# Kernel tuning notes

Hardware: AMD Instinct MI355X
Metric: run time of the kernel (lower is better)

The kernel has to match this reference:

```python
import jax, jax.numpy as jnp
import numpy as np

LN_EPS = 1e-5
L2_EPS = 1e-12
SCALE = 8.0

def setup_inputs() -> dict:
    key = jax.random.key(0)
    k0, k1, k2 = jax.random.split(key, 3)
    b, c, H, W = 16, 256, 64, 64
    heads, dim_head = 8, 32
    dim_inner = heads * dim_head  # 256
    x = jax.random.normal(k0, (b, c, H, W), dtype=jnp.float32)
    ln_gamma = jnp.ones((c,), jnp.float32)
    ln_beta = jnp.zeros((c,), jnp.float32)
    W_qkv = jax.random.normal(k1, (c, 3 * dim_inner), dtype=jnp.float32) * 0.02
    temperature = jnp.ones((heads,), jnp.float32)
    W_out = jax.random.normal(k2, (dim_inner, c), dtype=jnp.float32) * 0.02
    b_out = jnp.zeros((c,), jnp.float32)
    return {"x": x, "ln_gamma": ln_gamma, "ln_beta": ln_beta, "W_qkv": W_qkv,
            "temperature": temperature, "W_out": W_out, "b_out": b_out, "heads": heads}

def _l2norm(t):
    # F.normalize(t, dim=-1): divide by clamped L2 norm along last axis
    n = jnp.sqrt(jnp.sum(t * t, axis=-1, keepdims=True))
    return t / jnp.maximum(n, L2_EPS)

def reference(x, ln_gamma, ln_beta, W_qkv, temperature, W_out, b_out, heads):
    b, c, H, W = x.shape
    n = H * W
    dim_head = W_qkv.shape[1] // (3 * heads)
    # b c h w -> b (h w) c
    t = jnp.transpose(x, (0, 2, 3, 1)).reshape(b, n, c)
    # LayerNorm over channel dim (affine)
    mu = jnp.mean(t, axis=-1, keepdims=True)
    var = jnp.mean(jnp.square(t - mu), axis=-1, keepdims=True)
    t = (t - mu) * jax.lax.rsqrt(var + LN_EPS) * ln_gamma + ln_beta
    # qkv projection; split last dim as (qkv, heads, dim_head) -> (3, b, h, d, n)
    qkv = (t @ W_qkv).reshape(b, n, 3, heads, dim_head)
    qkv = jnp.transpose(qkv, (2, 0, 3, 4, 1))
    q, k, v = qkv[0], qkv[1], qkv[2]
    q = _l2norm(q) * jnp.exp(temperature)[None, :, None, None]
    k = _l2norm(k)
    # cross-covariance attention over channel dim: sim is [b, h, d, d]
    sim = jnp.einsum('bhin,bhjn->bhij', q, k) * SCALE
    attn = jax.nn.softmax(sim, axis=-1)
    out = jnp.einsum('bhij,bhjn->bhin', attn, v)  # [b, h, d, n]
    # b h d n -> b n (h d)
    out = jnp.transpose(out, (0, 3, 1, 2)).reshape(b, n, heads * dim_head)
    out = out @ W_out + b_out
    # b (h w) c -> b c h w
    return jnp.transpose(out.reshape(b, H, W, c), (0, 3, 1, 2))
```

## Files before the change

### kernel.cpp

```cpp
#include <hip/hip_runtime.h>

typedef unsigned short u16;
typedef __bf16 bf16x8 __attribute__((ext_vector_type(8)));
typedef float f32x4 __attribute__((ext_vector_type(4)));

#define MFMA(a, b, c) __builtin_amdgcn_mfma_f32_16x16x32_bf16((a), (b), (c), 0, 0, 0)

__device__ __forceinline__ u16 f2bf(float f) {
    unsigned u = __float_as_uint(f);
    unsigned r = (u + 0x7fffu + ((u >> 16) & 1u)) >> 16;
    return (u16)r;
}
__device__ __forceinline__ float bf2f(u16 h) { return __uint_as_float(((unsigned)h) << 16); }

typedef unsigned int u32_g __attribute__((address_space(1)));
typedef unsigned int u32_l __attribute__((address_space(3)));
__device__ __forceinline__ void gload16(const void* g, void* l) {
    __builtin_amdgcn_global_load_lds((const u32_g*)g, (u32_l*)l, 16, 0, 0);
}


__global__ __launch_bounds__(256) void k_ln(const float* __restrict__ x,
                                            const float* __restrict__ gamma,
                                            const float* __restrict__ beta,
                                            u16* __restrict__ xlnT, u16* __restrict__ xcn) {
    int bid = blockIdx.x;
    int b = bid >> 7, nt = bid & 127;
    int nb = nt * 32;
    __shared__ float redS[32 * 17], redS2[32 * 17];
    __shared__ float muv[32], rsv[32];
    __shared__ float gs[256], es[256];
    __shared__ unsigned xst[256 * 17];
    int t = threadIdx.x;
    int np = t & 15, cg = t >> 4;
    gs[t] = gamma[t];
    es[t] = beta[t];
    const float* xp = x + ((size_t)(b * 256 + cg * 16)) * 4096 + nb + np * 2;
    float2 v[16];
    float s0 = 0.f, s1 = 0.f, s20 = 0.f, s21 = 0.f;
#pragma unroll
    for (int i = 0; i < 16; i++) {
        float2 f = *(const float2*)(xp + (size_t)i * 4096);
        v[i] = f;
        s0 += f.x; s20 += f.x * f.x;
        s1 += f.y; s21 += f.y * f.y;
    }
    redS[(2 * np) * 17 + cg] = s0;
    redS[(2 * np + 1) * 17 + cg] = s1;
    redS2[(2 * np) * 17 + cg] = s20;
    redS2[(2 * np + 1) * 17 + cg] = s21;
    __syncthreads();
    if (t < 32) {
        float s = 0.f, s2 = 0.f;
#pragma unroll
        for (int g = 0; g < 16; g++) { s += redS[t * 17 + g]; s2 += redS2[t * 17 + g]; }
        float m = s * (1.f / 256.f);
        float var = s2 * (1.f / 256.f) - m * m;
        muv[t] = m;
        rsv[t] = rsqrtf(var + 1e-5f);
    }
    __syncthreads();
    float m0 = muv[2 * np], r0 = rsv[2 * np];
    float m1 = muv[2 * np + 1], r1 = rsv[2 * np + 1];
    u16 hA[16], hB[16];
#pragma unroll
    for (int i = 0; i < 16; i++) {
        float g = gs[cg * 16 + i], e = es[cg * 16 + i];
        float a = (v[i].x - m0) * r0 * g + e;
        float c2 = (v[i].y - m1) * r1 * g + e;
        u16 ha = f2bf(a), hb = f2bf(c2);
        hA[i] = ha; hB[i] = hb;
        xst[(cg * 16 + i) * 17 + np] = (unsigned)ha | ((unsigned)hb << 16);
    }
    {
        u16* dst0 = xlnT + ((size_t)(b * 4096 + nb + 2 * np)) * 256 + cg * 16;
        uint4 qa, qb;
        qa.x = (unsigned)hA[0] | ((unsigned)hA[1] << 16);
        qa.y = (unsigned)hA[2] | ((unsigned)hA[3] << 16);
        qa.z = (unsigned)hA[4] | ((unsigned)hA[5] << 16);
        qa.w = (unsigned)hA[6] | ((unsigned)hA[7] << 16);
        qb.x = (unsigned)hA[8] | ((unsigned)hA[9] << 16);
        qb.y = (unsigned)hA[10] | ((unsigned)hA[11] << 16);
        qb.z = (unsigned)hA[12] | ((unsigned)hA[13] << 16);
        qb.w = (unsigned)hA[14] | ((unsigned)hA[15] << 16);
        *(uint4*)dst0 = qa;
        *(uint4*)(dst0 + 8) = qb;
        u16* dst1 = dst0 + 256;
        qa.x = (unsigned)hB[0] | ((unsigned)hB[1] << 16);
        qa.y = (unsigned)hB[2] | ((unsigned)hB[3] << 16);
        qa.z = (unsigned)hB[4] | ((unsigned)hB[5] << 16);
        qa.w = (unsigned)hB[6] | ((unsigned)hB[7] << 16);
        qb.x = (unsigned)hB[8] | ((unsigned)hB[9] << 16);
        qb.y = (unsigned)hB[10] | ((unsigned)hB[11] << 16);
        qb.z = (unsigned)hB[12] | ((unsigned)hB[13] << 16);
        qb.w = (unsigned)hB[14] | ((unsigned)hB[15] << 16);
        *(uint4*)dst1 = qa;
        *(uint4*)(dst1 + 8) = qb;
    }
    __syncthreads();
#pragma unroll
    for (int j = 0; j < 4; j++) {
        int row = (t >> 2) + j * 64, part = t & 3;
        uint4 q;
        q.x = xst[row * 17 + part * 4 + 0];
        q.y = xst[row * 17 + part * 4 + 1];
        q.z = xst[row * 17 + part * 4 + 2];
        q.w = xst[row * 17 + part * 4 + 3];
        *(uint4*)(xcn + ((size_t)(b * 256 + row)) * 4096 + nb + part * 8) = q;
    }
}

__global__ __launch_bounds__(256) void k_prep(const float* __restrict__ Wqkv,
                                              const float* __restrict__ Wout,
                                              u16* __restrict__ WqkvT, u16* __restrict__ WvTn,
                                              u16* __restrict__ WoutT) {
    int i = blockIdx.x * 256 + threadIdx.x;
    if (i < 512 * 256) { int o = i >> 8, c = i & 255; WqkvT[i] = f2bf(Wqkv[c * 768 + o]); }
    if (i < 256 * 256) {
        int e = i >> 8, o = i & 255;
        WvTn[i] = f2bf(Wqkv[e * 768 + 512 + o]);
        WoutT[i] = f2bf(Wout[o * 256 + e]);
    }
}

__global__ __launch_bounds__(256) void k_gram(const u16* __restrict__ xcn, float* __restrict__ Gp) {
    int bid = blockIdx.x;
    int s = bid & 7, tile = (bid >> 3) & 3, b = bid >> 5;
    int tm = tile >> 1, tn = tile & 1;
    __shared__ __align__(16) u16 aT[128 * 32];
    __shared__ __align__(16) u16 bT[128 * 32];
    int t = threadIdx.x, w = t >> 6, lane = t & 63, l15 = lane & 15, quad = lane >> 4;
    int srow = lane >> 2;
    int g8 = (((lane & 3) ^ ((lane >> 3) & 3)) << 3);
    const u16* xb = xcn + (size_t)b * 256 * 4096 + (size_t)s * 512;
    const u16* gA = xb + (size_t)(tm * 128 + w * 32 + srow) * 4096 + g8;
    const u16* gB = xb + (size_t)(tn * 128 + w * 32 + srow) * 4096 + g8;
    u16* lA = aT + w * 1024;
    u16* lB = bT + w * 1024;
    int cOff = ((quad ^ ((l15 >> 1) & 3)) << 3);
    f32x4 acc[2][8];
    f32x4 z = {0.f, 0.f, 0.f, 0.f};
    for (int fm = 0; fm < 2; fm++)
        for (int fn = 0; fn < 8; fn++) acc[fm][fn] = z;
    for (int kt = 0; kt < 16; kt++) {
        int kb = kt * 32;
        if (kt) __syncthreads();
        gload16(gA + kb, lA);
        gload16(gA + 16 * 4096 + kb, lA + 512);
        gload16(gB + kb, lB);
        gload16(gB + 16 * 4096 + kb, lB + 512);
        __syncthreads();
        bf16x8 af0 = *(const bf16x8*)&aT[(w * 32 + l15) * 32 + cOff];
        bf16x8 af1 = *(const bf16x8*)&aT[(w * 32 + 16 + l15) * 32 + cOff];
        for (int fn = 0; fn < 8; fn++) {
            bf16x8 bfr = *(const bf16x8*)&bT[(fn * 16 + l15) * 32 + cOff];
            acc[0][fn] = MFMA(af0, bfr, acc[0][fn]);
            acc[1][fn] = MFMA(af1, bfr, acc[1][fn]);
        }
    }
    float* gp = Gp + (size_t)(s * 16 + b) * 65536;
    for (int fm = 0; fm < 2; fm++)
        for (int fn = 0; fn < 8; fn++)
            for (int r = 0; r < 4; r++) {
                int row = tm * 128 + w * 32 + fm * 16 + quad * 4 + r;
                int col = tn * 128 + fn * 16 + l15;
                gp[row * 256 + col] = acc[fm][fn][r];
            }
}

__global__ __launch_bounds__(256) void k_g2b(const float* __restrict__ Gp,
                                             u16* __restrict__ Ghi, u16* __restrict__ Glo) {
    int idx = blockIdx.x * 256 + threadIdx.x;
    const float4* p = (const float4*)Gp + idx;
    float4 s = p[0];
#pragma unroll
    for (int j = 1; j < 8; j++) {
        float4 v = p[(size_t)j * 262144];
        s.x += v.x; s.y += v.y; s.z += v.z; s.w += v.w;
    }
    u16 h0 = f2bf(s.x), h1 = f2bf(s.y), h2 = f2bf(s.z), h3 = f2bf(s.w);
    u16 l0 = f2bf(s.x - bf2f(h0)), l1 = f2bf(s.y - bf2f(h1));
    u16 l2 = f2bf(s.z - bf2f(h2)), l3 = f2bf(s.w - bf2f(h3));
    uint2 ph; ph.x = (unsigned)h0 | ((unsigned)h1 << 16); ph.y = (unsigned)h2 | ((unsigned)h3 << 16);
    uint2 pl; pl.x = (unsigned)l0 | ((unsigned)l1 << 16); pl.y = (unsigned)l2 | ((unsigned)l3 << 16);
    *(uint2*)(Ghi + (size_t)idx * 4) = ph;
    *(uint2*)(Glo + (size_t)idx * 4) = pl;
}

__global__ __launch_bounds__(256) void k_sq(const u16* __restrict__ A,
                                            const u16* __restrict__ Ghi, const u16* __restrict__ Glo,
                                            u16* __restrict__ Shi, u16* __restrict__ Slo) {
    __shared__ __align__(16) u16 aT[128 * 32];
    __shared__ __align__(16) u16 bT[128 * 32];
    int bid = blockIdx.x;
    int b = bid >> 3;
    int r2 = bid & 7;
    int mbase = (r2 >> 1) * 128, nbase = (r2 & 1) * 128;
    int t = threadIdx.x, w = t >> 6, lane = t & 63, l15 = lane & 15, quad = lane >> 4;
    int srow = lane >> 2;
    int g8 = (((lane & 3) ^ ((lane >> 3) & 3)) << 3);
    const u16* gA = A + (size_t)(mbase + w * 32 + srow) * 256 + g8;
    const u16* gBh = Ghi + (size_t)b * 65536 + (size_t)(nbase + w * 32 + srow) * 256 + g8;
    const u16* gBl = Glo + (size_t)b * 65536 + (size_t)(nbase + w * 32 + srow) * 256 + g8;
    u16* lA = aT + w * 1024;
    u16* lB = bT + w * 1024;
    int cOff = ((quad ^ ((l15 >> 1) & 3)) << 3);
    f32x4 acc[2][8];
    f32x4 z = {0.f, 0.f, 0.f, 0.f};
    for (int fm = 0; fm < 2; fm++)
        for (int fn = 0; fn < 8; fn++) acc[fm][fn] = z;
    for (int kt = 0; kt < 16; kt++) {
        int kb = (kt & 7) * 32;
        const u16* gB = (kt < 8) ? gBh : gBl;
        if (kt) __syncthreads();
        gload16(gA + kb, lA);
        gload16(gA + 16 * 256 + kb, lA + 512);
        gload16(gB + kb, lB);
        gload16(gB + 16 * 256 + kb, lB + 512);
        __syncthreads();
        bf16x8 af0 = *(const bf16x8*)&aT[(w * 32 + l15) * 32 + cOff];
        bf16x8 af1 = *(const bf16x8*)&aT[(w * 32 + 16 + l15) * 32 + cOff];
        for (int fn = 0; fn < 8; fn++) {
            bf16x8 bfr = *(const bf16x8*)&bT[(fn * 16 + l15) * 32 + cOff];
            acc[0][fn] = MFMA(af0, bfr, acc[0][fn]);
            acc[1][fn] = MFMA(af1, bfr, acc[1][fn]);
        }
    }
    for (int fm = 0; fm < 2; fm++)
        for (int fn = 0; fn < 8; fn++)
            for (int r = 0; r < 4; r++) {
                int row = mbase + w * 32 + fm * 16 + quad * 4 + r;
                int col = nbase + fn * 16 + l15;
                float v = acc[fm][fn][r];
                u16 hi = f2bf(v);
                Shi[((size_t)b * 512 + row) * 256 + col] = hi;
                Slo[((size_t)b * 512 + row) * 256 + col] = f2bf(v - bf2f(hi));
            }
}

__global__ __launch_bounds__(256) void k_gemm(const u16* __restrict__ A, size_t aStrB,
                                              const u16* __restrict__ Bb, size_t bStrB,
                                              int mtiles, int ntiles,
                                              u16* __restrict__ o16, float* __restrict__ o32,
                                              const float* __restrict__ bias,
                                              size_t oStrB, int oRstr, int mode) {
    __shared__ __align__(16) u16 aT[128 * 32];
    __shared__ __align__(16) u16 bT[128 * 32];
    int bid = blockIdx.x;
    int per_b = mtiles * ntiles;
    int b = bid / per_b;
    int r2 = bid % per_b;
    int mbase = (r2 / ntiles) * 128, nbase = (r2 % ntiles) * 128;
    int t = threadIdx.x, w = t >> 6, lane = t & 63, l15 = lane & 15, quad = lane >> 4;
    const u16* Ap = A + (size_t)b * aStrB;
    const u16* Bp = Bb + (size_t)b * bStrB;
    int srow = lane >> 2;
    int g8 = (((lane & 3) ^ ((lane >> 3) & 3)) << 3);
    const u16* gA = Ap + (size_t)(mbase + w * 32 + srow) * 256 + g8;
    const u16* gB = Bp + (size_t)(nbase + w * 32 + srow) * 256 + g8;
    u16* lA = aT + w * 1024;
    u16* lB = bT + w * 1024;
    int cOff = ((quad ^ ((l15 >> 1) & 3)) << 3);
    f32x4 acc[2][8];
    f32x4 z = {0.f, 0.f, 0.f, 0.f};
    for (int fm = 0; fm < 2; fm++)
        for (int fn = 0; fn < 8; fn++) acc[fm][fn] = z;
    for (int kt = 0; kt < 8; kt++) {
        int kb = kt * 32;
        if (kt) __syncthreads();
        gload16(gA + kb, lA);
        gload16(gA + 16 * 256 + kb, lA + 512);
        gload16(gB + kb, lB);
        gload16(gB + 16 * 256 + kb, lB + 512);
        __syncthreads();
        bf16x8 af0 = *(const bf16x8*)&aT[(w * 32 + l15) * 32 + cOff];
        bf16x8 af1 = *(const bf16x8*)&aT[(w * 32 + 16 + l15) * 32 + cOff];
        for (int fn = 0; fn < 8; fn++) {
            bf16x8 bfr = *(const bf16x8*)&bT[(fn * 16 + l15) * 32 + cOff];
            acc[0][fn] = MFMA(af0, bfr, acc[0][fn]);
            acc[1][fn] = MFMA(af1, bfr, acc[1][fn]);
        }
    }
    if (mode == 0) {
        for (int fm = 0; fm < 2; fm++)
            for (int fn = 0; fn < 8; fn++)
                for (int r = 0; r < 4; r++) {
                    int row = mbase + w * 32 + fm * 16 + quad * 4 + r;
                    int col = nbase + fn * 16 + l15;
                    o16[(size_t)b * oStrB + (size_t)row * oRstr + col] = f2bf(acc[fm][fn][r]);
                }
    } else {
        for (int fm = 0; fm < 2; fm++)
            for (int fn = 0; fn < 8; fn++)
                for (int r = 0; r < 4; r++) {
                    int row = mbase + w * 32 + fm * 16 + quad * 4 + r;
                    int col = nbase + fn * 16 + l15;
                    o32[(size_t)b * oStrB + (size_t)row * oRstr + col] = acc[fm][fn][r] + bias[row];
                }
    }
}

__global__ __launch_bounds__(256) void k_attn(const u16* __restrict__ Shi,
                                              const u16* __restrict__ Slo,
                                              const u16* __restrict__ WqkvT,
                                              const u16* __restrict__ WoutT,
                                              const float* __restrict__ temp,
                                              u16* __restrict__ M_all) {
    int bh = blockIdx.x;
    int b = bh >> 3, h = bh & 7;
    __shared__ u16 sqh[32 * 264], sql[32 * 264], skh[32 * 264], wq[32 * 264], wk[32 * 264];
    __shared__ u16 wo[256 * 40];
    __shared__ u16 attnT[32 * 40];
    __shared__ float simS[32 * 33];
    __shared__ float redn[4 * 64];
    __shared__ float scq[32], sck[32];
    int t = threadIdx.x, w = t >> 6, lane = t & 63, l15 = lane & 15, quad = lane >> 4;
    {
        int r = t >> 3, cc0 = (t & 7) * 32;
        const u16* gqh = Shi + ((size_t)(b * 512) + h * 32 + r) * 256 + cc0;
        const u16* gql = Slo + ((size_t)(b * 512) + h * 32 + r) * 256 + cc0;
        const u16* gkh = Shi + ((size_t)(b * 512) + 256 + h * 32 + r) * 256 + cc0;
        const u16* gwq = WqkvT + (size_t)(h * 32 + r) * 256 + cc0;
        const u16* gwk = WqkvT + (size_t)(256 + h * 32 + r) * 256 + cc0;
#pragma unroll
        for (int k = 0; k < 4; k++) {
            *(uint4*)&sqh[r * 264 + cc0 + k * 8] = *(const uint4*)(gqh + k * 8);
            *(uint4*)&sql[r * 264 + cc0 + k * 8] = *(const uint4*)(gql + k * 8);
            *(uint4*)&skh[r * 264 + cc0 + k * 8] = *(const uint4*)(gkh + k * 8);
            *(uint4*)&wq[r * 264 + cc0 + k * 8] = *(const uint4*)(gwq + k * 8);
            *(uint4*)&wk[r * 264 + cc0 + k * 8] = *(const uint4*)(gwk + k * 8);
        }
        const u16* gwo = WoutT + (size_t)t * 256 + h * 32;
#pragma unroll
        for (int k = 0; k < 4; k++) *(uint4*)&wo[t * 40 + k * 8] = *(const uint4*)(gwo + k * 8);
    }
    __syncthreads();
    {
        int rn = t & 63, cc = t >> 6;
        int e0 = cc * 64;
        float s = 0.f;
        if (rn < 32) {
            const u16* ph = &sqh[rn * 264];
            const u16* pl = &sql[rn * 264];
            const u16* pb = &wq[rn * 264];
            for (int e = 0; e < 64; e++)
                s += (bf2f(ph[e0 + e]) + bf2f(pl[e0 + e])) * bf2f(pb[e0 + e]);
        } else {
            const u16* ph = &skh[(rn - 32) * 264];
            const u16* pb = &wk[(rn - 32) * 264];
            for (int e = 0; e < 64; e++)
                s += bf2f(ph[e0 + e]) * bf2f(pb[e0 + e]);
        }
        redn[cc * 64 + rn] = s;
    }
    {
        int iq = w >> 1, jq = w & 1;
        f32x4 acc = {0.f, 0.f, 0.f, 0.f};
        for (int s8 = 0; s8 < 8; s8++) {
            bf16x8 a = *(const bf16x8*)&sqh[(iq * 16 + l15) * 264 + s8 * 32 + quad * 8];
            bf16x8 bb = *(const bf16x8*)&wk[(jq * 16 + l15) * 264 + s8 * 32 + quad * 8];
            acc = MFMA(a, bb, acc);
        }
        for (int s8 = 0; s8 < 8; s8++) {
            bf16x8 a = *(const bf16x8*)&sql[(iq * 16 + l15) * 264 + s8 * 32 + quad * 8];
            bf16x8 bb = *(const bf16x8*)&wk[(jq * 16 + l15) * 264 + s8 * 32 + quad * 8];
            acc = MFMA(a, bb, acc);
        }
        for (int r = 0; r < 4; r++)
            simS[(iq * 16 + quad * 4 + r) * 33 + jq * 16 + l15] = acc[r];
    }
    __syncthreads();
    if (t < 32)
        scq[t] = expf(temp[h]) * 8.0f /
                 fmaxf(sqrtf(redn[t] + redn[64 + t] + redn[128 + t] + redn[192 + t]), 1e-12f);
    else if (t < 64) {
        int d = t - 32;
        sck[d] = 1.0f / fmaxf(sqrtf(redn[32 + d] + redn[96 + d] + redn[160 + d] + redn[224 + d]), 1e-12f);
    }
    __syncthreads();
    if (t < 32) {
        float row[32];
        float m = -1e30f, sqv = scq[t];
#pragma unroll
        for (int j = 0; j < 32; j++) {
            float v = simS[t * 33 + j] * sqv * sck[j];
            row[j] = v; m = fmaxf(m, v);
        }
        float s = 0.f;
#pragma unroll
        for (int j = 0; j < 32; j++) { float p = expf(row[j] - m); row[j] = p; s += p; }
        float inv = 1.f / s;
#pragma unroll
        for (int j = 0; j < 32; j++) attnT[j * 40 + t] = f2bf(row[j] * inv);
    }
    __syncthreads();
    {
        f32x4 z = {0.f, 0.f, 0.f, 0.f};
        for (int mf = 0; mf < 4; mf++) {
            bf16x8 a = *(const bf16x8*)&wo[((w * 4 + mf) * 16 + l15) * 40 + quad * 8];
            for (int nf = 0; nf < 2; nf++) {
                bf16x8 bb = *(const bf16x8*)&attnT[(nf * 16 + l15) * 40 + quad * 8];
                f32x4 d = MFMA(a, bb, z);
                for (int r = 0; r < 4; r++) {
                    int c = (w * 4 + mf) * 16 + quad * 4 + r;
                    M_all[((size_t)(b * 256) + c) * 256 + h * 32 + nf * 16 + l15] = f2bf(d[r]);
                }
            }
        }
    }
}

extern "C" void kernel_launch(void* const* d_in, const int* in_sizes, int n_in,
                              void* d_out, int out_size, void* d_ws, size_t ws_size,
                              hipStream_t stream) {
    const float* x     = (const float*)d_in[0];
    const float* gamma = (const float*)d_in[1];
    const float* beta  = (const float*)d_in[2];
    const float* Wqkv  = (const float*)d_in[3];
    const float* temp  = (const float*)d_in[4];
    const float* Wout  = (const float*)d_in[5];
    const float* bout  = (const float*)d_in[6];
    float* out = (float*)d_out;

    char* ws = (char*)d_ws;
    size_t off = 0;
    auto alloc = [&](size_t nbytes) -> void* {
        void* p = ws + off;
        off = (off + nbytes + 255) & ~(size_t)255;
        return p;
    };
    u16* xlnT   = (u16*)alloc((size_t)16 * 4096 * 256 * 2);
    u16* xcn    = (u16*)alloc((size_t)16 * 256 * 4096 * 2);
    u16* WqkvT  = (u16*)alloc((size_t)512 * 256 * 2);
    u16* WvTn   = (u16*)alloc((size_t)256 * 256 * 2);
    u16* WoutT  = (u16*)alloc((size_t)256 * 256 * 2);
    float* Gp   = (float*)alloc((size_t)8 * 16 * 65536 * 4);
    u16* Gbh    = (u16*)alloc((size_t)16 * 65536 * 2);
    u16* Gbl    = (u16*)alloc((size_t)16 * 65536 * 2);
    u16* Sqh    = (u16*)alloc((size_t)16 * 512 * 256 * 2);
    u16* Sql    = (u16*)alloc((size_t)16 * 512 * 256 * 2);
    u16* M_all  = (u16*)alloc((size_t)16 * 256 * 256 * 2);
    u16* F      = (u16*)alloc((size_t)16 * 256 * 256 * 2);
    (void)ws_size; (void)in_sizes; (void)n_in; (void)out_size;

    hipLaunchKernelGGL(k_ln, dim3(2048), dim3(256), 0, stream, x, gamma, beta, xlnT, xcn);
    hipLaunchKernelGGL(k_prep, dim3(768), dim3(256), 0, stream, Wqkv, Wout, WqkvT, WvTn, WoutT);
    hipLaunchKernelGGL(k_gram, dim3(512), dim3(256), 0, stream, xcn, Gp);
    hipLaunchKernelGGL(k_g2b, dim3(1024), dim3(256), 0, stream, Gp, Gbh, Gbl);
    hipLaunchKernelGGL(k_sq, dim3(128), dim3(256), 0, stream, WqkvT, Gbh, Gbl, Sqh, Sql);
    hipLaunchKernelGGL(k_attn, dim3(128), dim3(256), 0, stream, Sqh, Sql, WqkvT, WoutT, temp, M_all);
    hipLaunchKernelGGL(k_gemm, dim3(64), dim3(256), 0, stream,
                       M_all, (size_t)65536, WvTn, (size_t)0, 2, 2,
                       F, (float*)nullptr, (const float*)nullptr,
                       (size_t)65536, 256, 0);
    hipLaunchKernelGGL(k_gemm, dim3(1024), dim3(256), 0, stream,
                       F, (size_t)65536, xlnT, (size_t)4096 * 256, 2, 32,
                       (u16*)nullptr, out, bout,
                       (size_t)256 * 4096, 4096, 1);
}
```

Before: 224.3 us.

## Fuse LayerNorm with Gram accumulation via atomics and add dedicated output GEMM kernel

LayerNorm and the channel Gram matrix computation now live in one 1024-thread kernel. Each block normalizes a 128-position chunk into swizzled LDS, runs MFMA on it, and atomically adds its partial Gram into a single fp32 buffer that k_prep zeroes. This drops the xcn transposed intermediate, the 8-way split partial buffer and the reduction in k_g2b, which cuts global traffic. A new k_out kernel with 256x128 tiles replaces the generic output GEMM, giving fewer blocks and more A reuse. The cost is heavy fp32 atomic contention (32 blocks per batch hit the same 64K entries) and summation order that is no longer deterministic.

```diff
diff --git a/kernel.cpp b/kernel.cpp
--- a/kernel.cpp
+++ b/kernel.cpp
@@ -20,21 +20,17 @@
 }
 
 
-__global__ __launch_bounds__(256) void k_ln(const float* __restrict__ x,
-                                            const float* __restrict__ gamma,
-                                            const float* __restrict__ beta,
-                                            u16* __restrict__ xlnT, u16* __restrict__ xcn) {
+__global__ __launch_bounds__(1024) void k_lngram(const float* __restrict__ x,
+                                                 const float* __restrict__ gamma,
+                                                 const float* __restrict__ beta,
+                                                 u16* __restrict__ xlnT, float* __restrict__ Gf) {
+    __shared__ __align__(16) unsigned smem[256 * 64];
+    float* sf = (float*)smem;
     int bid = blockIdx.x;
-    int b = bid >> 7, nt = bid & 127;
-    int nb = nt * 32;
-    __shared__ float redS[32 * 17], redS2[32 * 17];
-    __shared__ float muv[32], rsv[32];
-    __shared__ float gs[256], es[256];
-    __shared__ unsigned xst[256 * 17];
+    int b = bid >> 5, ch = bid & 31;
+    int nb = ch * 128;
     int t = threadIdx.x;
-    int np = t & 15, cg = t >> 4;
-    gs[t] = gamma[t];
-    es[t] = beta[t];
+    int np = t & 63, cg = t >> 6;
     const float* xp = x + ((size_t)(b * 256 + cg * 16)) * 4096 + nb + np * 2;
     float2 v[16];
     float s0 = 0.f, s1 = 0.f, s20 = 0.f, s21 = 0.f;
@@ -45,33 +41,38 @@
         s0 += f.x; s20 += f.x * f.x;
         s1 += f.y; s21 += f.y * f.y;
     }
-    redS[(2 * np) * 17 + cg] = s0;
-    redS[(2 * np + 1) * 17 + cg] = s1;
-    redS2[(2 * np) * 17 + cg] = s20;
-    redS2[(2 * np + 1) * 17 + cg] = s21;
-    __syncthreads();
-    if (t < 32) {
+    sf[cg * 128 + 2 * np] = s0;
+    sf[cg * 128 + 2 * np + 1] = s1;
+    sf[2048 + cg * 128 + 2 * np] = s20;
+    sf[2048 + cg * 128 + 2 * np + 1] = s21;
+    __syncthreads();
+    if (t < 128) {
         float s = 0.f, s2 = 0.f;
 #pragma unroll
-        for (int g = 0; g < 16; g++) { s += redS[t * 17 + g]; s2 += redS2[t * 17 + g]; }
+        for (int g = 0; g < 16; g++) { s += sf[g * 128 + t]; s2 += sf[2048 + g * 128 + t]; }
         float m = s * (1.f / 256.f);
         float var = s2 * (1.f / 256.f) - m * m;
-        muv[t] = m;
-        rsv[t] = rsqrtf(var + 1e-5f);
-    }
-    __syncthreads();
-    float m0 = muv[2 * np], r0 = rsv[2 * np];
-    float m1 = muv[2 * np + 1], r1 = rsv[2 * np + 1];
+        sf[4096 + t] = m;
+        sf[4224 + t] = rsqrtf(var + 1e-5f);
+    }
+    __syncthreads();
+    float m0 = sf[4096 + 2 * np], r0 = sf[4224 + 2 * np];
+    float m1 = sf[4096 + 2 * np + 1], r1 = sf[4224 + 2 * np + 1];
+    __syncthreads();
     u16 hA[16], hB[16];
+    int sw = ((np >> 2) ^ (cg & 15));
 #pragma unroll
     for (int i = 0; i < 16; i++) {
-        float g = gs[cg * 16 + i], e = es[cg * 16 + i];
+        int c = cg * 16 + i;
+        float g = gamma[c], e = beta[c];
         float a = (v[i].x - m0) * r0 * g + e;
-        float c2 = (v[i].y - m1) * r1 * g + e;
-        u16 ha = f2bf(a), hb = f2bf(c2);
+        float bv = (v[i].y - m1) * r1 * g + e;
+        u16 ha = f2bf(a), hb = f2bf(bv);
         hA[i] = ha; hB[i] = hb;
-        xst[(cg * 16 + i) * 17 + np] = (unsigned)ha | ((unsigned)hb << 16);
-    }
+        int dw = c * 64 + ((((np >> 2) ^ (c & 15)) << 2) | (np & 3));
+        smem[dw] = (unsigned)ha | ((unsigned)hb << 16);
+    }
+    (void)sw;
     {
         u16* dst0 = xlnT + ((size_t)(b * 4096 + nb + 2 * np)) * 256 + cg * 16;
         uint4 qa, qb;
@@ -98,22 +99,43 @@
         *(uint4*)(dst1 + 8) = qb;
     }
     __syncthreads();
-#pragma unroll
-    for (int j = 0; j < 4; j++) {
-        int row = (t >> 2) + j * 64, part = t & 3;
-        uint4 q;
-        q.x = xst[row * 17 + part * 4 + 0];
-        q.y = xst[row * 17 + part * 4 + 1];
-        q.z = xst[row * 17 + part * 4 + 2];
-        q.w = xst[row * 17 + part * 4 + 3];
-        *(uint4*)(xcn + ((size_t)(b * 256 + row)) * 4096 + nb + part * 8) = q;
+    {
+        int lane = t & 63, l15 = lane & 15, quad = lane >> 4;
+        int w = t >> 6;
+        int mr2 = (w & 7) * 2, nf0 = (w >> 3) * 8;
+        f32x4 acc[2][8];
+        f32x4 z = {0.f, 0.f, 0.f, 0.f};
+        for (int fm = 0; fm < 2; fm++)
+            for (int j = 0; j < 8; j++) acc[fm][j] = z;
+#pragma unroll
+        for (int ks = 0; ks < 4; ks++) {
+            int ca0 = (mr2 * 16 + l15);
+            int ca1 = ((mr2 + 1) * 16 + l15);
+            bf16x8 a0 = *(const bf16x8*)&smem[ca0 * 64 + (((ks * 4 + quad) ^ (ca0 & 15)) << 2)];
+            bf16x8 a1 = *(const bf16x8*)&smem[ca1 * 64 + (((ks * 4 + quad) ^ (ca1 & 15)) << 2)];
+#pragma unroll
+            for (int j = 0; j < 8; j++) {
+                int cb = ((nf0 + j) * 16 + l15);
+                bf16x8 bb = *(const bf16x8*)&smem[cb * 64 + (((ks * 4 + quad) ^ (cb & 15)) << 2)];
+                acc[0][j] = MFMA(a0, bb, acc[0][j]);
+                acc[1][j] = MFMA(a1, bb, acc[1][j]);
+            }
+        }
+        float* gp = Gf + (size_t)b * 65536;
+        for (int fm = 0; fm < 2; fm++)
+            for (int j = 0; j < 8; j++)
+                for (int r = 0; r < 4; r++) {
+                    int row = (mr2 + fm) * 16 + quad * 4 + r;
+                    int col = (nf0 + j) * 16 + l15;
+                    atomicAdd(gp + row * 256 + col, acc[fm][j][r]);
+                }
     }
 }
 
 __global__ __launch_bounds__(256) void k_prep(const float* __restrict__ Wqkv,
                                               const float* __restrict__ Wout,
                                               u16* __restrict__ WqkvT, u16* __restrict__ WvTn,
-                                              u16* __restrict__ WoutT) {
+                                              u16* __restrict__ WoutT, float* __restrict__ Gf) {
     int i = blockIdx.x * 256 + threadIdx.x;
     if (i < 512 * 256) { int o = i >> 8, c = i & 255; WqkvT[i] = f2bf(Wqkv[c * 768 + o]); }
     if (i < 256 * 256) {
@@ -121,63 +143,14 @@
         WvTn[i] = f2bf(Wqkv[e * 768 + 512 + o]);
         WoutT[i] = f2bf(Wout[o * 256 + e]);
     }
-}
-
-__global__ __launch_bounds__(256) void k_gram(const u16* __restrict__ xcn, float* __restrict__ Gp) {
-    int bid = blockIdx.x;
-    int s = bid & 7, tile = (bid >> 3) & 3, b = bid >> 5;
-    int tm = tile >> 1, tn = tile & 1;
-    __shared__ __align__(16) u16 aT[128 * 32];
-    __shared__ __align__(16) u16 bT[128 * 32];
-    int t = threadIdx.x, w = t >> 6, lane = t & 63, l15 = lane & 15, quad = lane >> 4;
-    int srow = lane >> 2;
-    int g8 = (((lane & 3) ^ ((lane >> 3) & 3)) << 3);
-    const u16* xb = xcn + (size_t)b * 256 * 4096 + (size_t)s * 512;
-    const u16* gA = xb + (size_t)(tm * 128 + w * 32 + srow) * 4096 + g8;
-    const u16* gB = xb + (size_t)(tn * 128 + w * 32 + srow) * 4096 + g8;
-    u16* lA = aT + w * 1024;
-    u16* lB = bT + w * 1024;
-    int cOff = ((quad ^ ((l15 >> 1) & 3)) << 3);
-    f32x4 acc[2][8];
-    f32x4 z = {0.f, 0.f, 0.f, 0.f};
-    for (int fm = 0; fm < 2; fm++)
-        for (int fn = 0; fn < 8; fn++) acc[fm][fn] = z;
-    for (int kt = 0; kt < 16; kt++) {
-        int kb = kt * 32;
-        if (kt) __syncthreads();
-        gload16(gA + kb, lA);
-        gload16(gA + 16 * 4096 + kb, lA + 512);
-        gload16(gB + kb, lB);
-        gload16(gB + 16 * 4096 + kb, lB + 512);
-        __syncthreads();
-        bf16x8 af0 = *(const bf16x8*)&aT[(w * 32 + l15) * 32 + cOff];
-        bf16x8 af1 = *(const bf16x8*)&aT[(w * 32 + 16 + l15) * 32 + cOff];
-        for (int fn = 0; fn < 8; fn++) {
-            bf16x8 bfr = *(const bf16x8*)&bT[(fn * 16 + l15) * 32 + cOff];
-            acc[0][fn] = MFMA(af0, bfr, acc[0][fn]);
-            acc[1][fn] = MFMA(af1, bfr, acc[1][fn]);
-        }
-    }
-    float* gp = Gp + (size_t)(s * 16 + b) * 65536;
-    for (int fm = 0; fm < 2; fm++)
-        for (int fn = 0; fn < 8; fn++)
-            for (int r = 0; r < 4; r++) {
-                int row = tm * 128 + w * 32 + fm * 16 + quad * 4 + r;
-                int col = tn * 128 + fn * 16 + l15;
-                gp[row * 256 + col] = acc[fm][fn][r];
-            }
-}
-
-__global__ __launch_bounds__(256) void k_g2b(const float* __restrict__ Gp,
+    float4 z4 = {0.f, 0.f, 0.f, 0.f};
+    if (i < 262144) ((float4*)Gf)[i] = z4;
+}
+
+__global__ __launch_bounds__(256) void k_g2b(const float* __restrict__ Gf,
                                              u16* __restrict__ Ghi, u16* __restrict__ Glo) {
     int idx = blockIdx.x * 256 + threadIdx.x;
-    const float4* p = (const float4*)Gp + idx;
-    float4 s = p[0];
-#pragma unroll
-    for (int j = 1; j < 8; j++) {
-        float4 v = p[(size_t)j * 262144];
-        s.x += v.x; s.y += v.y; s.z += v.z; s.w += v.w;
-    }
+    float4 s = ((const float4*)Gf)[idx];
     u16 h0 = f2bf(s.x), h1 = f2bf(s.y), h2 = f2bf(s.z), h3 = f2bf(s.w);
     u16 l0 = f2bf(s.x - bf2f(h0)), l1 = f2bf(s.y - bf2f(h1));
     u16 l2 = f2bf(s.z - bf2f(h2)), l3 = f2bf(s.w - bf2f(h3));
@@ -300,6 +273,54 @@
     }
 }
 
+__global__ __launch_bounds__(256) void k_out(const u16* __restrict__ F, const u16* __restrict__ xlnT,
+                                             const float* __restrict__ bias, float* __restrict__ out) {
+    __shared__ __align__(16) u16 aT[256 * 32];
+    __shared__ __align__(16) u16 bT[128 * 32];
+    int bid = blockIdx.x;
+    int b = bid >> 5, nt = bid & 31;
+    int nbase = nt * 128;
+    int t = threadIdx.x, w = t >> 6, lane = t & 63, l15 = lane & 15, quad = lane >> 4;
+    int srow = lane >> 2;
+    int g8 = (((lane & 3) ^ ((lane >> 3) & 3)) << 3);
+    const u16* gA = F + (size_t)b * 65536 + (size_t)(w * 64 + srow) * 256 + g8;
+    const u16* gB = xlnT + (size_t)b * 4096 * 256 + (size_t)(nbase + w * 32 + srow) * 256 + g8;
+    u16* lA = aT + w * 2048;
+    u16* lB = bT + w * 1024;
+    int cOff = ((quad ^ ((l15 >> 1) & 3)) << 3);
+    f32x4 acc[4][8];
+    f32x4 z = {0.f, 0.f, 0.f, 0.f};
+    for (int fm = 0; fm < 4; fm++)
+        for (int fn = 0; fn < 8; fn++) acc[fm][fn] = z;
+    for (int kt = 0; kt < 8; kt++) {
+        int kb = kt * 32;
+        if (kt) __syncthreads();
+        gload16(gA + kb, lA);
+        gload16(gA + 16 * 256 + kb, lA + 512);
+        gload16(gA + 32 * 256 + kb, lA + 1024);
+        gload16(gA + 48 * 256 + kb, lA + 1536);
+        gload16(gB + kb, lB);
+        gload16(gB + 16 * 256 + kb, lB + 512);
+        __syncthreads();
+        bf16x8 af[4];
+#pragma unroll
+        for (int fm = 0; fm < 4; fm++)
+            af[fm] = *(const bf16x8*)&aT[(w * 64 + fm * 16 + l15) * 32 + cOff];
+        for (int fn = 0; fn < 8; fn++) {
+            bf16x8 bfr = *(const bf16x8*)&bT[(fn * 16 + l15) * 32 + cOff];
+#pragma unroll
+            for (int fm = 0; fm < 4; fm++) acc[fm][fn] = MFMA(af[fm], bfr, acc[fm][fn]);
+        }
+    }
+    for (int fm = 0; fm < 4; fm++)
+        for (int fn = 0; fn < 8; fn++)
+            for (int r = 0; r < 4; r++) {
+                int row = w * 64 + fm * 16 + quad * 4 + r;
+                int col = nbase + fn * 16 + l15;
+                out[((size_t)b * 256 + row) * 4096 + col] = acc[fm][fn][r] + bias[row];
+            }
+}
+
 __global__ __launch_bounds__(256) void k_attn(const u16* __restrict__ Shi,
                                               const u16* __restrict__ Slo,
                                               const u16* __restrict__ WqkvT,
@@ -430,11 +451,10 @@
         return p;
     };
     u16* xlnT   = (u16*)alloc((size_t)16 * 4096 * 256 * 2);
-    u16* xcn    = (u16*)alloc((size_t)16 * 256 * 4096 * 2);
     u16* WqkvT  = (u16*)alloc((size_t)512 * 256 * 2);
     u16* WvTn   = (u16*)alloc((size_t)256 * 256 * 2);
     u16* WoutT  = (u16*)alloc((size_t)256 * 256 * 2);
-    float* Gp   = (float*)alloc((size_t)8 * 16 * 65536 * 4);
+    float* Gf   = (float*)alloc((size_t)16 * 65536 * 4);
     u16* Gbh    = (u16*)alloc((size_t)16 * 65536 * 2);
     u16* Gbl    = (u16*)alloc((size_t)16 * 65536 * 2);
     u16* Sqh    = (u16*)alloc((size_t)16 * 512 * 256 * 2);
@@ -443,18 +463,14 @@
     u16* F      = (u16*)alloc((size_t)16 * 256 * 256 * 2);
     (void)ws_size; (void)in_sizes; (void)n_in; (void)out_size;
 
-    hipLaunchKernelGGL(k_ln, dim3(2048), dim3(256), 0, stream, x, gamma, beta, xlnT, xcn);
-    hipLaunchKernelGGL(k_prep, dim3(768), dim3(256), 0, stream, Wqkv, Wout, WqkvT, WvTn, WoutT);
-    hipLaunchKernelGGL(k_gram, dim3(512), dim3(256), 0, stream, xcn, Gp);
-    hipLaunchKernelGGL(k_g2b, dim3(1024), dim3(256), 0, stream, Gp, Gbh, Gbl);
+    hipLaunchKernelGGL(k_prep, dim3(1024), dim3(256), 0, stream, Wqkv, Wout, WqkvT, WvTn, WoutT, Gf);
+    hipLaunchKernelGGL(k_lngram, dim3(512), dim3(1024), 0, stream, x, gamma, beta, xlnT, Gf);
+    hipLaunchKernelGGL(k_g2b, dim3(1024), dim3(256), 0, stream, Gf, Gbh, Gbl);
     hipLaunchKernelGGL(k_sq, dim3(128), dim3(256), 0, stream, WqkvT, Gbh, Gbl, Sqh, Sql);
     hipLaunchKernelGGL(k_attn, dim3(128), dim3(256), 0, stream, Sqh, Sql, WqkvT, WoutT, temp, M_all);
     hipLaunchKernelGGL(k_gemm, dim3(64), dim3(256), 0, stream,
                        M_all, (size_t)65536, WvTn, (size_t)0, 2, 2,
                        F, (float*)nullptr, (const float*)nullptr,
                        (size_t)65536, 256, 0);
-    hipLaunchKernelGGL(k_gemm, dim3(1024), dim3(256), 0, stream,
-                       F, (size_t)65536, xlnT, (size_t)4096 * 256, 2, 32,
-                       (u16*)nullptr, out, bout,
-                       (size_t)256 * 4096, 4096, 1);
-}
+    hipLaunchKernelGGL(k_out, dim3(512), dim3(256), 0, stream, F, xlnT, bout, out);
+}
```

Measured after the change: 276.0 us. 23.1% more time.
